# Optimization experiments

Hardware: AMD Instinct MI355X
Metric: run time of the kernel (lower is better)

The kernel has to match this reference:

```python
import jax, jax.numpy as jnp
import numpy as np

MAX_DISP = 4  # init kwarg


def setup_inputs() -> dict:
    key = jax.random.key(0)
    k1, k2 = jax.random.split(key)
    x_1 = jax.random.normal(k1, (8, 128, 128, 128), dtype=jnp.float32)
    x_2 = jax.random.normal(k2, (8, 128, 128, 128), dtype=jnp.float32)
    return {"x_1": x_1, "x_2": x_2}


def reference(x_1, x_2):
    d = MAX_DISP
    H, W = x_1.shape[2], x_1.shape[3]
    # zero-pad x_2 by max_disp on both spatial dims (ConstantPad2d)
    x2p = jnp.pad(x_2, ((0, 0), (0, 0), (d, d), (d, d)))
    # loop over the fixed (2d+1)^2 = 81 displacement offsets (structural, not data dim)
    outs = [
        jnp.mean(x_1 * x2p[:, :, dx:dx + H, dy:dy + W], axis=1)  # [B,H,W]
        for dx in range(2 * d + 1)
        for dy in range(2 * d + 1)
    ]
    return jnp.stack(outs, axis=1)  # [B, 81, H, W]
```

## Files before the change

### kernel.cpp

```cpp
#include <hip/hip_runtime.h>


constexpr int Cn = 128, Hn = 128, Wn = 128;
constexpr int HWn = Hn * Wn;
constexpr int TH = 4;
constexpr int NROWS = 16;
constexpr int ROWF  = 128;
constexpr int CHF   = NROWS * ROWF;
constexpr int BUFF  = 2 * CHF;

__device__ __forceinline__ float dpp_shr1(float x) {
  return __int_as_float(__builtin_amdgcn_update_dpp(
      0, __float_as_int(x), 0x111, 0xF, 0xF, true));
}
__device__ __forceinline__ float dpp_shl1(float x) {
  return __int_as_float(__builtin_amdgcn_update_dpp(
      0, __float_as_int(x), 0x101, 0xF, 0xF, true));
}

__global__ __launch_bounds__(576, 3)
void corr_kernel(const float* __restrict__ x1, const float* __restrict__ x2,
                 float* __restrict__ out) {
  __shared__ float lds[2][2][NROWS][ROWF];

  const int t    = threadIdx.x;
  const int w    = t >> 6;
  const int lane = t & 63;
  const int r    = lane >> 4;
  const int l    = lane & 15;

  const int phys = blockIdx.x;
  const int b    = phys & 7;
  const int tile = phys >> 3;
  const int h0   = tile * TH;
  const int dh   = w - 4;

  const bool stg  = t < 512;
  const int ridx  = t >> 5;
  const int s     = t & 31;
  const int j     = (s < 16) ? (s << 1) : (((s - 16) << 1) | 1);
  int gr;
  bool okg;
  if (ridx < 4) { gr = h0 + ridx; okg = true; }
  else { gr = h0 + ridx - 8; okg = (unsigned)gr < (unsigned)Hn; }
  const float* src = (ridx < 4 ? x1 : x2) + (size_t)b * Cn * HWn
                   + (size_t)(okg ? gr : 0) * Wn + (j << 2);
  okg = okg && stg;
  float* const L = &lds[0][0][0][0];
  const int woff = ridx * ROWF + (s << 2);

  const int rx  = r + dh + 8;
  const int o1l = r * ROWF + (l << 2);
  const int o1h = o1l + 64;
  const int o2l = rx * ROWF + (l << 2);
  const int o2h = o2l + 64;

  float4 acc0[9], acc1[9];
#pragma unroll
  for (int dw = 0; dw < 9; ++dw) {
    acc0[dw] = make_float4(0.f, 0.f, 0.f, 0.f);
    acc1[dw] = make_float4(0.f, 0.f, 0.f, 0.f);
  }

  const float4 z4 = make_float4(0.f, 0.f, 0.f, 0.f);
  float4 pv0 = z4, pv1 = z4;
  if (okg) { pv0 = *(const float4*)src; pv1 = *(const float4*)(src + HWn); }
  src += 2 * HWn;

#pragma unroll 1
  for (int step = 0; step < 64; ++step) {
    const int bo = (step & 1) * BUFF;
    if (stg) {
      *(float4*)(L + bo + woff)       = pv0;
      *(float4*)(L + bo + CHF + woff) = pv1;
    }
    __syncthreads();
    if (okg && step < 63) {
      pv0 = *(const float4*)src;
      pv1 = *(const float4*)(src + HWn);
    }
    src += 2 * HWn;

#pragma unroll
    for (int ch = 0; ch < 2; ++ch) {
      const float* p = L + bo + ch * CHF;
      const float4 a0 = *(const float4*)(p + o1l);
      const float4 a1 = *(const float4*)(p + o1h);
      const float4 b0 = *(const float4*)(p + o2l);
      const float4 b1 = *(const float4*)(p + o2h);
      const float win[16] = {
          dpp_shr1(b1.x), dpp_shr1(b1.y), dpp_shr1(b1.z), dpp_shr1(b1.w),
          b0.x, b0.y, b0.z, b0.w,
          b1.x, b1.y, b1.z, b1.w,
          dpp_shl1(b0.x), dpp_shl1(b0.y), dpp_shl1(b0.z), dpp_shl1(b0.w)};
      const float av[8] = {a0.x, a0.y, a0.z, a0.w, a1.x, a1.y, a1.z, a1.w};
#pragma unroll
      for (int dw = 0; dw < 9; ++dw) {
        acc0[dw].x += av[0] * win[dw + 0];
        acc0[dw].y += av[1] * win[dw + 1];
        acc0[dw].z += av[2] * win[dw + 2];
        acc0[dw].w += av[3] * win[dw + 3];
        acc1[dw].x += av[4] * win[dw + 4];
        acc1[dw].y += av[5] * win[dw + 5];
        acc1[dw].z += av[6] * win[dw + 6];
        acc1[dw].w += av[7] * win[dw + 7];
      }
    }
  }

  const float scale = 1.0f / 128.0f;
  float* ob = out + ((size_t)b * 81 + (size_t)w * 9) * HWn
                  + (size_t)(h0 + r) * Wn + (l << 3);
#pragma unroll
  for (int dw = 0; dw < 9; ++dw) {
    float4 r0, r1;
    r0.x = acc0[dw].x * scale; r0.y = acc0[dw].y * scale;
    r0.z = acc0[dw].z * scale; r0.w = acc0[dw].w * scale;
    r1.x = acc1[dw].x * scale; r1.y = acc1[dw].y * scale;
    r1.z = acc1[dw].z * scale; r1.w = acc1[dw].w * scale;
    *(float4*)(ob + (size_t)dw * HWn)     = r0;
    *(float4*)(ob + (size_t)dw * HWn + 4) = r1;
  }
}

extern "C" void kernel_launch(void* const* d_in, const int* in_sizes, int n_in,
                              void* d_out, int out_size, void* d_ws, size_t ws_size,
                              hipStream_t stream) {
  const float* x1 = (const float*)d_in[0];
  const float* x2 = (const float*)d_in[1];
  float* out = (float*)d_out;
  const int n_wgs = 8 * (Hn / TH);
  corr_kernel<<<dim3(n_wgs), dim3(576), 0, stream>>>(x1, x2, out);
}
```

Measured before the change: 177.7 us.

## Split vertical displacements across two smaller workgroups per tile

Each 4-row tile is now handled by two 320-thread workgroups: one covers vertical displacements 0-4 with five waves, the other covers 5-8 with four active waves. The grid doubles from 256 to 512 workgroups, and each workgroup stages a smaller 12-row LDS window, which raises parallelism and occupancy. The cost is that x1 and the overlapping x2 rows are loaded twice, one wave in the second kind idles, and there are more barriers in total.

Result: slower. 224.7 us (+26.4%).

```diff
diff --git a/kernel.cpp b/kernel.cpp
--- a/kernel.cpp
+++ b/kernel.cpp
@@ -4,7 +4,7 @@
 constexpr int Cn = 128, Hn = 128, Wn = 128;
 constexpr int HWn = Hn * Wn;
 constexpr int TH = 4;
-constexpr int NROWS = 16;
+constexpr int NROWS = 12;
 constexpr int ROWF  = 128;
 constexpr int CHF   = NROWS * ROWF;
 constexpr int BUFF  = 2 * CHF;
@@ -18,7 +18,7 @@
       0, __float_as_int(x), 0x101, 0xF, 0xF, true));
 }
 
-__global__ __launch_bounds__(576, 3)
+__global__ __launch_bounds__(320, 3)
 void corr_kernel(const float* __restrict__ x1, const float* __restrict__ x2,
                  float* __restrict__ out) {
   __shared__ float lds[2][2][NROWS][ROWF];
@@ -31,28 +31,37 @@
 
   const int phys = blockIdx.x;
   const int b    = phys & 7;
-  const int tile = phys >> 3;
+  const int slot = phys >> 3;
+  const int kind = slot & 1;
+  const int tile = slot >> 1;
   const int h0   = tile * TH;
-  const int dh   = w - 4;
 
-  const bool stg  = t < 512;
-  const int ridx  = t >> 5;
-  const int s     = t & 31;
-  const int j     = (s < 16) ? (s << 1) : (((s - 16) << 1) | 1);
-  int gr;
-  bool okg;
-  if (ridx < 4) { gr = h0 + ridx; okg = true; }
-  else { gr = h0 + ridx - 8; okg = (unsigned)gr < (unsigned)Hn; }
-  const float* src = (ridx < 4 ? x1 : x2) + (size_t)b * Cn * HWn
-                   + (size_t)(okg ? gr : 0) * Wn + (j << 2);
-  okg = okg && stg;
+  const int ridx = t >> 5;
+  const int s    = t & 31;
+  const int j    = (s < 16) ? (s << 1) : (((s - 16) << 1) | 1);
+  int grP; bool okP; const float* baseP;
+  if (ridx < 4) { grP = h0 + ridx; okP = true; baseP = x1; }
+  else { grP = h0 + ridx - 8 + 5 * kind; okP = ((unsigned)grP < (unsigned)Hn); baseP = x2; }
+  const float* srcP = baseP + (size_t)b * Cn * HWn
+                    + (size_t)(okP ? grP : 0) * Wn + (j << 2);
+  const int woffP = ridx * ROWF + (s << 2);
+
+  const bool sec = t < 64;
+  const int ridx2 = 10 + (t >> 5);
+  const int grS  = h0 + ridx2 - 8 + 5 * kind;
+  const bool okS = sec && ((unsigned)grS < (unsigned)Hn);
+  const float* srcS = x2 + (size_t)b * Cn * HWn
+                    + (size_t)(okS ? grS : 0) * Wn + (j << 2);
+  const int woffS = ridx2 * ROWF + (s << 2);
+
   float* const L = &lds[0][0][0][0];
-  const int woff = ridx * ROWF + (s << 2);
 
-  const int rx  = r + dh + 8;
+  const bool active = (kind == 0) | (w < 4);
+  const int dhi = w + 5 * kind;
+  const int rxi = r + w + 4;
   const int o1l = r * ROWF + (l << 2);
   const int o1h = o1l + 64;
-  const int o2l = rx * ROWF + (l << 2);
+  const int o2l = rxi * ROWF + (l << 2);
   const int o2h = o2l + 64;
 
   float4 acc0[9], acc1[9];
@@ -63,63 +72,72 @@
   }
 
   const float4 z4 = make_float4(0.f, 0.f, 0.f, 0.f);
-  float4 pv0 = z4, pv1 = z4;
-  if (okg) { pv0 = *(const float4*)src; pv1 = *(const float4*)(src + HWn); }
-  src += 2 * HWn;
+  float4 pv0 = z4, pv1 = z4, pw0 = z4, pw1 = z4;
+  if (okP) { pv0 = *(const float4*)srcP; pv1 = *(const float4*)(srcP + HWn); }
+  if (okS) { pw0 = *(const float4*)srcS; pw1 = *(const float4*)(srcS + HWn); }
+  srcP += 2 * (size_t)HWn;
+  srcS += 2 * (size_t)HWn;
 
 #pragma unroll 1
   for (int step = 0; step < 64; ++step) {
     const int bo = (step & 1) * BUFF;
-    if (stg) {
-      *(float4*)(L + bo + woff)       = pv0;
-      *(float4*)(L + bo + CHF + woff) = pv1;
+    *(float4*)(L + bo + woffP)       = pv0;
+    *(float4*)(L + bo + CHF + woffP) = pv1;
+    if (sec) {
+      *(float4*)(L + bo + woffS)       = pw0;
+      *(float4*)(L + bo + CHF + woffS) = pw1;
     }
     __syncthreads();
-    if (okg && step < 63) {
-      pv0 = *(const float4*)src;
-      pv1 = *(const float4*)(src + HWn);
+    if (step < 63) {
+      if (okP) { pv0 = *(const float4*)srcP; pv1 = *(const float4*)(srcP + HWn); }
+      if (okS) { pw0 = *(const float4*)srcS; pw1 = *(const float4*)(srcS + HWn); }
     }
-    src += 2 * HWn;
+    srcP += 2 * (size_t)HWn;
+    srcS += 2 * (size_t)HWn;
 
+    if (active) {
 #pragma unroll
-    for (int ch = 0; ch < 2; ++ch) {
-      const float* p = L + bo + ch * CHF;
-      const float4 a0 = *(const float4*)(p + o1l);
-      const float4 a1 = *(const float4*)(p + o1h);
-      const float4 b0 = *(const float4*)(p + o2l);
-      const float4 b1 = *(const float4*)(p + o2h);
-      const float win[16] = {
-          dpp_shr1(b1.x), dpp_shr1(b1.y), dpp_shr1(b1.z), dpp_shr1(b1.w),
-          b0.x, b0.y, b0.z, b0.w,
-          b1.x, b1.y, b1.z, b1.w,
-          dpp_shl1(b0.x), dpp_shl1(b0.y), dpp_shl1(b0.z), dpp_shl1(b0.w)};
-      const float av[8] = {a0.x, a0.y, a0.z, a0.w, a1.x, a1.y, a1.z, a1.w};
+      for (int ch = 0; ch < 2; ++ch) {
+        const float* p = L + bo + ch * CHF;
+        const float4 a0 = *(const float4*)(p + o1l);
+        const float4 a1 = *(const float4*)(p + o1h);
+        const float4 b0 = *(const float4*)(p + o2l);
+        const float4 b1 = *(const float4*)(p + o2h);
+        const float win[16] = {
+            dpp_shr1(b1.x), dpp_shr1(b1.y), dpp_shr1(b1.z), dpp_shr1(b1.w),
+            b0.x, b0.y, b0.z, b0.w,
+            b1.x, b1.y, b1.z, b1.w,
+            dpp_shl1(b0.x), dpp_shl1(b0.y), dpp_shl1(b0.z), dpp_shl1(b0.w)};
+        const float av[8] = {a0.x, a0.y, a0.z, a0.w, a1.x, a1.y, a1.z, a1.w};
 #pragma unroll
-      for (int dw = 0; dw < 9; ++dw) {
-        acc0[dw].x += av[0] * win[dw + 0];
-        acc0[dw].y += av[1] * win[dw + 1];
-        acc0[dw].z += av[2] * win[dw + 2];
-        acc0[dw].w += av[3] * win[dw + 3];
-        acc1[dw].x += av[4] * win[dw + 4];
-        acc1[dw].y += av[5] * win[dw + 5];
-        acc1[dw].z += av[6] * win[dw + 6];
-        acc1[dw].w += av[7] * win[dw + 7];
+        for (int dw = 0; dw < 9; ++dw) {
+          acc0[dw].x += av[0] * win[dw + 0];
+          acc0[dw].y += av[1] * win[dw + 1];
+          acc0[dw].z += av[2] * win[dw + 2];
+          acc0[dw].w += av[3] * win[dw + 3];
+          acc1[dw].x += av[4] * win[dw + 4];
+          acc1[dw].y += av[5] * win[dw + 5];
+          acc1[dw].z += av[6] * win[dw + 6];
+          acc1[dw].w += av[7] * win[dw + 7];
+        }
       }
     }
   }
 
-  const float scale = 1.0f / 128.0f;
-  float* ob = out + ((size_t)b * 81 + (size_t)w * 9) * HWn
-                  + (size_t)(h0 + r) * Wn + (l << 3);
+  if (active) {
+    const float scale = 1.0f / 128.0f;
+    float* ob = out + ((size_t)b * 81 + (size_t)dhi * 9) * HWn
+                    + (size_t)(h0 + r) * Wn + (l << 3);
 #pragma unroll
-  for (int dw = 0; dw < 9; ++dw) {
-    float4 r0, r1;
-    r0.x = acc0[dw].x * scale; r0.y = acc0[dw].y * scale;
-    r0.z = acc0[dw].z * scale; r0.w = acc0[dw].w * scale;
-    r1.x = acc1[dw].x * scale; r1.y = acc1[dw].y * scale;
-    r1.z = acc1[dw].z * scale; r1.w = acc1[dw].w * scale;
-    *(float4*)(ob + (size_t)dw * HWn)     = r0;
-    *(float4*)(ob + (size_t)dw * HWn + 4) = r1;
+    for (int dw = 0; dw < 9; ++dw) {
+      float4 r0, r1;
+      r0.x = acc0[dw].x * scale; r0.y = acc0[dw].y * scale;
+      r0.z = acc0[dw].z * scale; r0.w = acc0[dw].w * scale;
+      r1.x = acc1[dw].x * scale; r1.y = acc1[dw].y * scale;
+      r1.z = acc1[dw].z * scale; r1.w = acc1[dw].w * scale;
+      *(float4*)(ob + (size_t)dw * HWn)     = r0;
+      *(float4*)(ob + (size_t)dw * HWn + 4) = r1;
+    }
   }
 }
 
@@ -129,6 +147,6 @@
   const float* x1 = (const float*)d_in[0];
   const float* x2 = (const float*)d_in[1];
   float* out = (float*)d_out;
-  const int n_wgs = 8 * (Hn / TH);
-  corr_kernel<<<dim3(n_wgs), dim3(576), 0, stream>>>(x1, x2, out);
+  const int n_wgs = 8 * (Hn / TH) * 2;
+  corr_kernel<<<dim3(n_wgs), dim3(320), 0, stream>>>(x1, x2, out);
 }
```

## Split each row tile's nine vertical displacements across three smaller workgroups

Applied to the files above, without the earlier changes.

Each 576-thread workgroup that computed all 9 vertical displacements for a 4-row tile is split into three 192-thread workgroups, each handling 3 vertical displacements and staging only 10 rows (4 of x1 plus 6 of x2) per channel in LDS. This triples the grid size and shrinks LDS per workgroup, aiming for better occupancy and load balance across CUs, with cheaper per-block barriers. The cost is that x1 rows and overlapping x2 rows are loaded three times from global memory, raising total read traffic.

Measured after the change: 184.2 us. 3.6% more time.

```diff
diff --git a/kernel.cpp b/kernel.cpp
--- a/kernel.cpp
+++ b/kernel.cpp
@@ -4,7 +4,7 @@
 constexpr int Cn = 128, Hn = 128, Wn = 128;
 constexpr int HWn = Hn * Wn;
 constexpr int TH = 4;
-constexpr int NROWS = 16;
+constexpr int NROWS = 10;
 constexpr int ROWF  = 128;
 constexpr int CHF   = NROWS * ROWF;
 constexpr int BUFF  = 2 * CHF;
@@ -18,7 +18,7 @@
       0, __float_as_int(x), 0x101, 0xF, 0xF, true));
 }
 
-__global__ __launch_bounds__(576, 3)
+__global__ __launch_bounds__(192, 3)
 void corr_kernel(const float* __restrict__ x1, const float* __restrict__ x2,
                  float* __restrict__ out) {
   __shared__ float lds[2][2][NROWS][ROWF];
@@ -31,28 +31,36 @@
 
   const int phys = blockIdx.x;
   const int b    = phys & 7;
-  const int tile = phys >> 3;
+  const int slot = phys >> 3;
+  const int tile = slot / 3;
+  const int g    = slot - tile * 3;
   const int h0   = tile * TH;
-  const int dh   = w - 4;
+  const int dhm  = g * 3 - 4;
 
-  const bool stg  = t < 512;
-  const int ridx  = t >> 5;
-  const int s     = t & 31;
-  const int j     = (s < 16) ? (s << 1) : (((s - 16) << 1) | 1);
-  int gr;
-  bool okg;
-  if (ridx < 4) { gr = h0 + ridx; okg = true; }
-  else { gr = h0 + ridx - 8; okg = (unsigned)gr < (unsigned)Hn; }
-  const float* src = (ridx < 4 ? x1 : x2) + (size_t)b * Cn * HWn
-                   + (size_t)(okg ? gr : 0) * Wn + (j << 2);
-  okg = okg && stg;
+  const int cA = t & 31, rowA = t >> 5;
+  const int jA = (cA < 16) ? (cA << 1) : (((cA - 16) << 1) | 1);
+  int grA; bool okA; const float* baseA;
+  if (rowA < 4) { grA = h0 + rowA; okA = true; baseA = x1; }
+  else { grA = h0 + dhm + rowA - 4; okA = ((unsigned)grA < (unsigned)Hn); baseA = x2; }
+  const float* srcA = baseA + (size_t)b * Cn * HWn
+                    + (size_t)(okA ? grA : 0) * Wn + (jA << 2);
+  const int woffA = t << 2;
+
+  const bool actB = t < 128;
+  const int sB = t + 192;
+  const int cB = sB & 31, rowB = sB >> 5;
+  const int jB = (cB < 16) ? (cB << 1) : (((cB - 16) << 1) | 1);
+  const int grB = h0 + dhm + rowB - 4;
+  const bool okB = actB && ((unsigned)grB < (unsigned)Hn);
+  const float* srcB = x2 + (size_t)b * Cn * HWn
+                    + (size_t)(okB ? grB : 0) * Wn + (jB << 2);
+  const int woffB = sB << 2;
+
   float* const L = &lds[0][0][0][0];
-  const int woff = ridx * ROWF + (s << 2);
 
-  const int rx  = r + dh + 8;
   const int o1l = r * ROWF + (l << 2);
   const int o1h = o1l + 64;
-  const int o2l = rx * ROWF + (l << 2);
+  const int o2l = (4 + r + w) * ROWF + (l << 2);
   const int o2h = o2l + 64;
 
   float4 acc0[9], acc1[9];
@@ -63,23 +71,28 @@
   }
 
   const float4 z4 = make_float4(0.f, 0.f, 0.f, 0.f);
-  float4 pv0 = z4, pv1 = z4;
-  if (okg) { pv0 = *(const float4*)src; pv1 = *(const float4*)(src + HWn); }
-  src += 2 * HWn;
+  float4 pvA0 = z4, pvA1 = z4, pvB0 = z4, pvB1 = z4;
+  if (okA) { pvA0 = *(const float4*)srcA; pvA1 = *(const float4*)(srcA + HWn); }
+  if (okB) { pvB0 = *(const float4*)srcB; pvB1 = *(const float4*)(srcB + HWn); }
+  srcA += 2 * (size_t)HWn;
+  srcB += 2 * (size_t)HWn;
 
 #pragma unroll 1
   for (int step = 0; step < 64; ++step) {
     const int bo = (step & 1) * BUFF;
-    if (stg) {
-      *(float4*)(L + bo + woff)       = pv0;
-      *(float4*)(L + bo + CHF + woff) = pv1;
+    *(float4*)(L + bo + woffA)       = pvA0;
+    *(float4*)(L + bo + CHF + woffA) = pvA1;
+    if (actB) {
+      *(float4*)(L + bo + woffB)       = pvB0;
+      *(float4*)(L + bo + CHF + woffB) = pvB1;
     }
     __syncthreads();
-    if (okg && step < 63) {
-      pv0 = *(const float4*)src;
-      pv1 = *(const float4*)(src + HWn);
+    if (step < 63) {
+      if (okA) { pvA0 = *(const float4*)srcA; pvA1 = *(const float4*)(srcA + HWn); }
+      if (okB) { pvB0 = *(const float4*)srcB; pvB1 = *(const float4*)(srcB + HWn); }
     }
-    src += 2 * HWn;
+    srcA += 2 * (size_t)HWn;
+    srcB += 2 * (size_t)HWn;
 
 #pragma unroll
     for (int ch = 0; ch < 2; ++ch) {
@@ -109,7 +122,8 @@
   }
 
   const float scale = 1.0f / 128.0f;
-  float* ob = out + ((size_t)b * 81 + (size_t)w * 9) * HWn
+  const int dhi = g * 3 + w;
+  float* ob = out + ((size_t)b * 81 + (size_t)dhi * 9) * HWn
                   + (size_t)(h0 + r) * Wn + (l << 3);
 #pragma unroll
   for (int dw = 0; dw < 9; ++dw) {
@@ -129,6 +143,6 @@
   const float* x1 = (const float*)d_in[0];
   const float* x2 = (const float*)d_in[1];
   float* out = (float*)d_out;
-  const int n_wgs = 8 * (Hn / TH);
-  corr_kernel<<<dim3(n_wgs), dim3(576), 0, stream>>>(x1, x2, out);
+  const int n_wgs = 8 * (Hn / TH) * 3;
+  corr_kernel<<<dim3(n_wgs), dim3(192), 0, stream>>>(x1, x2, out);
 }
```
